# Optimization experiments

Hardware: AMD Instinct MI355X
Metric: run time of the kernel (lower is better)

Reference implementation:

```python
import jax, jax.numpy as jnp
import numpy as np

B, P_LEN, Q_LEN, HID = 8, 2048, 1024, 1024


def setup_inputs() -> dict:
    key = jax.random.key(0)
    k1, k2, k3, k4 = jax.random.split(key, 4)
    k = jax.random.normal(k1, (B, P_LEN, HID), dtype=jnp.float32)
    q = jax.random.normal(k2, (B, Q_LEN, HID), dtype=jnp.float32)
    # q_mask: True = pad token. All-valid mask (no pads) to avoid NaN rows.
    q_mask = jnp.zeros((B, Q_LEN), dtype=bool)
    # Xavier-normal-initialized Linear weights, shape [out, in] as in torch.
    std = float(np.sqrt(2.0 / (HID + HID)))
    Wk = jax.random.normal(k3, (HID, HID), dtype=jnp.float32) * std
    Wq = jax.random.normal(k4, (HID, HID), dtype=jnp.float32) * std
    return {"k": k, "q": q, "q_mask": q_mask, "Wk": Wk, "Wq": Wq}


def reference(k, q, q_mask, Wk, Wq):
    # relu-projected keys/queries (Linear has no bias)
    p_key = jax.nn.relu(jnp.einsum('bpd,hd->bph', k, Wk))   # [B, p_len, hid]
    q_key = jax.nn.relu(jnp.einsum('bqd,hd->bqh', q, Wq))   # [B, q_len, hid]
    scores = jnp.einsum('bph,bqh->bpq', p_key, q_key)        # [B, p_len, q_len]
    scores = jnp.where(q_mask[:, None, :], -jnp.inf, scores)
    alphas = jax.nn.softmax(scores, axis=-1)                 # [B, p_len, q_len]
    ctx = jnp.einsum('bpq,bqd->bpd', alphas, q)              # [B, p_len, q_dim]
    return ctx, alphas
```

## Files before the change

kernel.cpp:

```cpp
#include <hip/hip_runtime.h>
#include <hip/hip_bf16.h>
#include <math.h>


typedef _Float16 v8h __attribute__((ext_vector_type(8)));
typedef _Float16 v4h __attribute__((ext_vector_type(4)));
typedef float v4f __attribute__((ext_vector_type(4)));

#define AS1C(p) ((const __attribute__((address_space(1))) void*)(p))
#define AS3(p)  ((__attribute__((address_space(3))) void*)(p))
#define MFMA16 __builtin_amdgcn_mfma_f32_16x16x32_f16

__global__ __launch_bounds__(512) void fused_attn(
    const _Float16* __restrict__ k16,
    const _Float16* __restrict__ Wk16,
    const _Float16* __restrict__ qkey16,
    const _Float16* __restrict__ qT16,
    const unsigned char* __restrict__ qmask,
    float* __restrict__ ctx,
    float* __restrict__ alphas)
{
  extern __shared__ _Float16 lds[];
  _Float16* Pk   = lds;
  _Float16* Sbuf = lds + 65536;
  float*    red1 = (float*)(lds + 73728);
  float*    red2 = (float*)(lds + 74752);

  const int bz   = blockIdx.x & 7;
  const int pblk = blockIdx.x >> 3;
  const int p0   = pblk * 64;

  const int t  = threadIdx.x;
  const int l  = t & 63;
  const int w  = t >> 6;
  const int fr = l & 15;
  const int fq = l >> 4;
  const int w128 = w * 128;
  const int sa0 = (fq ^ (fr & 7)) * 8;
  const int sa1 = ((4 + fq) ^ (fr & 7)) * 8;

  const int trow = t >> 3;
  const int tswz = ((t & 7) ^ (trow & 7)) * 8;

  const _Float16* Kst = k16 + ((long long)(bz * 2048 + p0 + trow)) * 1024 + tswz;
  const _Float16* qkb = qkey16 + (long long)bz * 1048576;
  const _Float16* qTb = qT16   + (long long)bz * 1048576;
  float* ctxb = ctx    + (long long)(bz * 2048 + p0) * 1024;
  float* alpb = alphas + (long long)(bz * 2048 + p0) * 1024;
  const unsigned char* mskb = qmask + bz * 1024;

  {
    v4f acc0[8][4];
#pragma unroll
    for (int i = 0; i < 8; ++i)
#pragma unroll
      for (int j = 0; j < 4; ++j)
        acc0[i][j] = (v4f){0.f, 0.f, 0.f, 0.f};

#define STAGE0(kt) __builtin_amdgcn_global_load_lds( \
      AS1C(Kst + ((long long)(kt) << 6)), AS3(Sbuf + (((kt) & 1) << 12) + t * 8), 16, 0, 0)

    STAGE0(0);
    for (int kt = 0; kt < 16; ++kt) {
      if (kt < 15) {
        STAGE0(kt + 1);
        asm volatile("s_waitcnt vmcnt(1)" ::: "memory");
      } else {
        asm volatile("s_waitcnt vmcnt(0)" ::: "memory");
      }
      __builtin_amdgcn_sched_barrier(0);
      __builtin_amdgcn_s_barrier();
      asm volatile("" ::: "memory");

      const _Float16* Bs = Sbuf + ((kt & 1) << 12);
      v8h b0[4], b1[4];
#pragma unroll
      for (int j = 0; j < 4; ++j) {
        b0[j] = *(const v8h*)&Bs[(j * 16 + fr) * 64 + sa0];
        b1[j] = *(const v8h*)&Bs[(j * 16 + fr) * 64 + sa1];
      }
#pragma unroll
      for (int i = 0; i < 8; ++i) {
        const v8h a0 = *(const v8h*)&Wk16[(long long)(w128 + i * 16 + fr) * 1024 + kt * 64 + fq * 8];
        const v8h a1 = *(const v8h*)&Wk16[(long long)(w128 + i * 16 + fr) * 1024 + kt * 64 + 32 + fq * 8];
#pragma unroll
        for (int j = 0; j < 4; ++j) {
          acc0[i][j] = MFMA16(a0, b0[j], acc0[i][j], 0, 0, 0);
          acc0[i][j] = MFMA16(a1, b1[j], acc0[i][j], 0, 0, 0);
        }
      }
      asm volatile("s_waitcnt lgkmcnt(0)" ::: "memory");
      __builtin_amdgcn_sched_barrier(0);
      __builtin_amdgcn_s_barrier();
    }
#undef STAGE0

#pragma unroll
    for (int i = 0; i < 8; ++i) {
#pragma unroll
      for (int j = 0; j < 4; ++j) {
        v4f v = acc0[i][j];
        v4h h4 = {(_Float16)fmaxf(v[0], 0.f), (_Float16)fmaxf(v[1], 0.f),
                  (_Float16)fmaxf(v[2], 0.f), (_Float16)fmaxf(v[3], 0.f)};
        const int p   = j * 16 + fr;
        const int s16 = w * 16 + i * 2 + (fq >> 1);
        const int phys = (s16 & ~7) | ((s16 & 7) ^ (p & 7));
        *(v4h*)&Pk[p * 1024 + phys * 8 + (fq & 1) * 4] = h4;
      }
    }
    __syncthreads();
  }

  float M4[4], IV[4];
  {
    v4f acc[8][4];
#pragma unroll
    for (int i = 0; i < 8; ++i)
#pragma unroll
      for (int j = 0; j < 4; ++j)
        acc[i][j] = (v4f){0.f, 0.f, 0.f, 0.f};

    for (int kt = 0; kt < 16; ++kt) {
      v8h pb0[4], pb1[4];
#pragma unroll
      for (int j = 0; j < 4; ++j) {
        pb0[j] = *(const v8h*)&Pk[(j * 16 + fr) * 1024 + kt * 64 + sa0];
        pb1[j] = *(const v8h*)&Pk[(j * 16 + fr) * 1024 + kt * 64 + sa1];
      }
#pragma unroll
      for (int i = 0; i < 8; ++i) {
        const v8h a0 = *(const v8h*)&qkb[(long long)(w128 + i * 16 + fr) * 1024 + kt * 64 + fq * 8];
        const v8h a1 = *(const v8h*)&qkb[(long long)(w128 + i * 16 + fr) * 1024 + kt * 64 + 32 + fq * 8];
#pragma unroll
        for (int j = 0; j < 4; ++j) {
          acc[i][j] = MFMA16(a0, pb0[j], acc[i][j], 0, 0, 0);
          acc[i][j] = MFMA16(a1, pb1[j], acc[i][j], 0, 0, 0);
        }
      }
    }

#pragma unroll
    for (int i = 0; i < 8; ++i) {
      const unsigned m4 = *(const unsigned*)&mskb[w128 + i * 16 + fq * 4];
      if (m4) {
#pragma unroll
        for (int r = 0; r < 4; ++r)
          if ((m4 >> (8 * r)) & 0xFF) {
#pragma unroll
            for (int j = 0; j < 4; ++j) acc[i][j][r] = -INFINITY;
          }
      }
    }

#pragma unroll
    for (int j = 0; j < 4; ++j) {
      float pm = -INFINITY;
#pragma unroll
      for (int i = 0; i < 8; ++i) {
        pm = fmaxf(pm, fmaxf(fmaxf(acc[i][j][0], acc[i][j][1]),
                             fmaxf(acc[i][j][2], acc[i][j][3])));
      }
      pm = fmaxf(pm, __shfl_xor(pm, 16, 64));
      pm = fmaxf(pm, __shfl_xor(pm, 32, 64));
      if (fq == 0) red1[(j * 16 + fr) * 8 + w] = pm;
    }
    __syncthreads();
#pragma unroll
    for (int j = 0; j < 4; ++j) {
      const float* r = &red1[(j * 16 + fr) * 8];
      M4[j] = fmaxf(fmaxf(fmaxf(r[0], r[1]), fmaxf(r[2], r[3])),
                    fmaxf(fmaxf(r[4], r[5]), fmaxf(r[6], r[7])));
    }

#pragma unroll
    for (int j = 0; j < 4; ++j) {
      float ps = 0.f;
#pragma unroll
      for (int i = 0; i < 8; ++i) {
#pragma unroll
        for (int r = 0; r < 4; ++r) {
          const float e = __expf(acc[i][j][r] - M4[j]);
          acc[i][j][r] = e;
          ps += e;
        }
      }
      ps += __shfl_xor(ps, 16, 64);
      ps += __shfl_xor(ps, 32, 64);
      if (fq == 0) red2[(j * 16 + fr) * 8 + w] = ps;
    }
    __syncthreads();
#pragma unroll
    for (int j = 0; j < 4; ++j) {
      const float* r = &red2[(j * 16 + fr) * 8];
      IV[j] = 1.f / (r[0] + r[1] + r[2] + r[3] + r[4] + r[5] + r[6] + r[7]);
    }

#pragma unroll
    for (int i = 0; i < 8; ++i) {
#pragma unroll
      for (int j = 0; j < 4; ++j) {
        float4 o;
        o.x = acc[i][j][0] * IV[j];
        o.y = acc[i][j][1] * IV[j];
        o.z = acc[i][j][2] * IV[j];
        o.w = acc[i][j][3] * IV[j];
        const int p = j * 16 + fr;
        *(float4*)&alpb[(long long)p * 1024 + w128 + i * 16 + fq * 4] = o;
        v4h h4 = {(_Float16)o.x, (_Float16)o.y, (_Float16)o.z, (_Float16)o.w};
        const int s16  = w * 16 + i * 2 + (fq >> 1);
        const int phys = (s16 & ~7) | ((s16 & 7) ^ (p & 7));
        *(v4h*)&Pk[p * 1024 + phys * 8 + (fq & 1) * 4] = h4;
      }
    }
    __syncthreads();
  }

  {
    v4f acc2[4][8];
#pragma unroll
    for (int i = 0; i < 4; ++i)
#pragma unroll
      for (int j = 0; j < 8; ++j)
        acc2[i][j] = (v4f){0.f, 0.f, 0.f, 0.f};

    for (int kt = 0; kt < 16; ++kt) {
      v8h pa0[4], pa1[4];
#pragma unroll
      for (int i = 0; i < 4; ++i) {
        pa0[i] = *(const v8h*)&Pk[(i * 16 + fr) * 1024 + kt * 64 + sa0];
        pa1[i] = *(const v8h*)&Pk[(i * 16 + fr) * 1024 + kt * 64 + sa1];
      }
#pragma unroll
      for (int j = 0; j < 8; ++j) {
        const v8h b0 = *(const v8h*)&qTb[(long long)(w128 + j * 16 + fr) * 1024 + kt * 64 + fq * 8];
        const v8h b1 = *(const v8h*)&qTb[(long long)(w128 + j * 16 + fr) * 1024 + kt * 64 + 32 + fq * 8];
#pragma unroll
        for (int i = 0; i < 4; ++i) {
          acc2[i][j] = MFMA16(pa0[i], b0, acc2[i][j], 0, 0, 0);
          acc2[i][j] = MFMA16(pa1[i], b1, acc2[i][j], 0, 0, 0);
        }
      }
    }

#pragma unroll
    for (int i = 0; i < 4; ++i) {
#pragma unroll
      for (int j = 0; j < 8; ++j) {
#pragma unroll
        for (int r = 0; r < 4; ++r) {
          ctxb[(long long)(i * 16 + fq * 4 + r) * 1024 + w128 + j * 16 + fr] = acc2[i][j][r];
        }
      }
    }
  }
}

__global__ __launch_bounds__(256) void gemm_nt_f16_128(
    const _Float16* __restrict__ A, const _Float16* __restrict__ B,
    float* __restrict__ Cf, _Float16* __restrict__ Ch,
    int N, int K, int Mtiles, int Ntiles,
    long long sA, long long sB, long long sC, int relu)
{
  extern __shared__ _Float16 lds[];

  const int nwg = gridDim.x;
  const int cpx = nwg >> 3;
  const int bid = (blockIdx.x & 7) * cpx + (blockIdx.x >> 3);
  const int nt  = bid % Ntiles;
  const int mt  = (bid / Ntiles) % Mtiles;
  const int bz  = bid / (Mtiles * Ntiles);

  A += (long long)bz * sA;
  const _Float16* Bp = B + (long long)bz * sB;

  const int m0 = mt * 128;
  const int n0 = nt * 128;
  const int t  = threadIdx.x;
  const int l  = t & 63;
  const int w  = t >> 6;
  const int wm = (w >> 1) * 64;
  const int wn = (w & 1) * 64;
  const int fr = l & 15;
  const int fq = l >> 4;
  const int r3 = fr & 7;
  const int sa0 = (fq ^ r3) * 8;
  const int sa1 = ((4 + fq) ^ r3) * 8;

  const int trow = t >> 3;
  const int tswz = ((t & 7) ^ (trow & 7)) * 8;

  const _Float16* Ast = A  + (long long)(m0 + trow) * K + tswz;
  const _Float16* Bst = Bp + (long long)(n0 + trow) * K + tswz;

  v4f acc[4][4];
#pragma unroll
  for (int i = 0; i < 4; ++i)
#pragma unroll
    for (int j = 0; j < 4; ++j)
      acc[i][j] = (v4f){0.f, 0.f, 0.f, 0.f};

  const int NT = K >> 6;

#define STAGE(kt) do {                                                                   \
    _Float16* s_ = lds + (((kt) & 1) << 14);                                             \
    const long long ko_ = (long long)((kt) << 6);                                        \
    __builtin_amdgcn_global_load_lds(AS1C(Ast + ko_),            AS3(s_ +         t * 8), 16, 0, 0); \
    __builtin_amdgcn_global_load_lds(AS1C(Ast + 32LL * K + ko_), AS3(s_ +  2048 + t * 8), 16, 0, 0); \
    __builtin_amdgcn_global_load_lds(AS1C(Ast + 64LL * K + ko_), AS3(s_ +  4096 + t * 8), 16, 0, 0); \
    __builtin_amdgcn_global_load_lds(AS1C(Ast + 96LL * K + ko_), AS3(s_ +  6144 + t * 8), 16, 0, 0); \
    __builtin_amdgcn_global_load_lds(AS1C(Bst + ko_),            AS3(s_ +  8192 + t * 8), 16, 0, 0); \
    __builtin_amdgcn_global_load_lds(AS1C(Bst + 32LL * K + ko_), AS3(s_ + 10240 + t * 8), 16, 0, 0); \
    __builtin_amdgcn_global_load_lds(AS1C(Bst + 64LL * K + ko_), AS3(s_ + 12288 + t * 8), 16, 0, 0); \
    __builtin_amdgcn_global_load_lds(AS1C(Bst + 96LL * K + ko_), AS3(s_ + 14336 + t * 8), 16, 0, 0); \
  } while (0)

  STAGE(0);

  for (int kt = 0; kt < NT; ++kt) {
    if (kt + 1 < NT) {
      STAGE(kt + 1);
      asm volatile("s_waitcnt vmcnt(8)" ::: "memory");
    } else {
      asm volatile("s_waitcnt vmcnt(0)" ::: "memory");
    }
    __builtin_amdgcn_sched_barrier(0);
    __builtin_amdgcn_s_barrier();
    asm volatile("" ::: "memory");

    const _Float16* Ab = lds + ((kt & 1) << 14);
    const _Float16* Bb = Ab + 8192;

    v8h a0[4], a1[4], b0[4], b1[4];
#pragma unroll
    for (int i = 0; i < 4; ++i) {
      a0[i] = *(const v8h*)&Ab[(wm + i * 16 + fr) * 64 + sa0];
      a1[i] = *(const v8h*)&Ab[(wm + i * 16 + fr) * 64 + sa1];
    }
#pragma unroll
    for (int j = 0; j < 2; ++j) {
      b0[j] = *(const v8h*)&Bb[(wn + j * 16 + fr) * 64 + sa0];
      b1[j] = *(const v8h*)&Bb[(wn + j * 16 + fr) * 64 + sa1];
    }
    __builtin_amdgcn_s_setprio(1);
#pragma unroll
    for (int i = 0; i < 4; ++i)
#pragma unroll
      for (int j = 0; j < 2; ++j) {
        acc[i][j] = MFMA16(a0[i], b0[j], acc[i][j], 0, 0, 0);
        acc[i][j] = MFMA16(a1[i], b1[j], acc[i][j], 0, 0, 0);
      }
    __builtin_amdgcn_s_setprio(0);

#pragma unroll
    for (int j = 2; j < 4; ++j) {
      b0[j] = *(const v8h*)&Bb[(wn + j * 16 + fr) * 64 + sa0];
      b1[j] = *(const v8h*)&Bb[(wn + j * 16 + fr) * 64 + sa1];
    }
    __builtin_amdgcn_s_setprio(1);
#pragma unroll
    for (int i = 0; i < 4; ++i)
#pragma unroll
      for (int j = 2; j < 4; ++j) {
        acc[i][j] = MFMA16(a0[i], b0[j], acc[i][j], 0, 0, 0);
        acc[i][j] = MFMA16(a1[i], b1[j], acc[i][j], 0, 0, 0);
      }
    __builtin_amdgcn_s_setprio(0);

    asm volatile("s_waitcnt lgkmcnt(0)" ::: "memory");
    __builtin_amdgcn_sched_barrier(0);
    __builtin_amdgcn_s_barrier();
  }
#undef STAGE

  float* Cfb = Cf ? Cf + (long long)bz * sC : nullptr;
  _Float16* Chb = Ch ? Ch + (long long)bz * sC : nullptr;
#pragma unroll
  for (int i = 0; i < 4; ++i) {
#pragma unroll
    for (int j = 0; j < 4; ++j) {
#pragma unroll
      for (int r = 0; r < 4; ++r) {
        const int row = m0 + wm + i * 16 + fq * 4 + r;
        const int col = n0 + wn + j * 16 + fr;
        float v = acc[i][j][r];
        if (relu) v = fmaxf(v, 0.f);
        if (Cfb) Cfb[(long long)row * N + col] = v;
        if (Chb) Chb[(long long)row * N + col] = (_Float16)v;
      }
    }
  }
}

__global__ __launch_bounds__(256) void convert_all_kernel(
    const float* __restrict__ s0, _Float16* __restrict__ d0, int b0,
    const float* __restrict__ s1, _Float16* __restrict__ d1, int b1,
    const float* __restrict__ s2, _Float16* __restrict__ d2, int b2,
    const float* __restrict__ s3, _Float16* __restrict__ d3)
{
  int blk = blockIdx.x;
  const float* src;
  _Float16* dst;
  if (blk < b0)           { src = s0; dst = d0; }
  else if (blk < b0 + b1) { src = s1; dst = d1; blk -= b0; }
  else if (blk < b0 + b1 + b2) { src = s2; dst = d2; blk -= b0 + b1; }
  else                    { src = s3; dst = d3; blk -= b0 + b1 + b2; }
  const long long i = ((long long)blk * 256 + threadIdx.x) * 4;
  const float4 v = *(const float4*)(src + i);
  v4h o = {(_Float16)v.x, (_Float16)v.y, (_Float16)v.z, (_Float16)v.w};
  *(v4h*)(dst + i) = o;
}

__global__ __launch_bounds__(256) void transpose_f16_kernel(
    const float* __restrict__ q, _Float16* __restrict__ qT, int Q, int H)
{
  __shared__ float tile[64][65];
  const float* qb = q + (long long)blockIdx.z * Q * H;
  _Float16* qTb = qT + (long long)blockIdx.z * H * Q;
  const int q0 = blockIdx.x * 64, h0 = blockIdx.y * 64;
  const int t = threadIdx.x;
  const int tr = t >> 4, tc = (t & 15) << 2;
#pragma unroll
  for (int i = 0; i < 4; ++i) {
    const float4 v = *(const float4*)(qb + (long long)(q0 + tr + i * 16) * H + h0 + tc);
    tile[tr + i * 16][tc + 0] = v.x;
    tile[tr + i * 16][tc + 1] = v.y;
    tile[tr + i * 16][tc + 2] = v.z;
    tile[tr + i * 16][tc + 3] = v.w;
  }
  __syncthreads();
#pragma unroll
  for (int i = 0; i < 4; ++i) {
    const int hl = tr + i * 16;
    const int ql = tc;
    v4h o = {(_Float16)tile[ql + 0][hl], (_Float16)tile[ql + 1][hl],
             (_Float16)tile[ql + 2][hl], (_Float16)tile[ql + 3][hl]};
    *(v4h*)(qTb + (long long)(h0 + hl) * Q + q0 + ql) = o;
  }
}

extern "C" void kernel_launch(void* const* d_in, const int* in_sizes, int n_in,
                              void* d_out, int out_size, void* d_ws, size_t ws_size,
                              hipStream_t stream)
{
  const int B = 8, P = 2048, Q = 1024, H = 1024;
  const float* k  = (const float*)d_in[0];
  const float* q  = (const float*)d_in[1];
  const unsigned char* qmask = (const unsigned char*)d_in[2];
  const float* Wk = (const float*)d_in[3];
  const float* Wq = (const float*)d_in[4];

  float* ctx    = (float*)d_out;
  float* alphas = ctx + (size_t)B * P * H;

  char* wsb = (char*)d_ws;
  _Float16* qkey16 = (_Float16*)(wsb);
  _Float16* k16    = (_Float16*)(wsb + 16777216);
  _Float16* q16    = (_Float16*)(wsb + 16777216 + 33554432);
  _Float16* qT16   = q16;
  _Float16* Wk16   = (_Float16*)(wsb + 67108864);
  _Float16* Wq16   = (_Float16*)(wsb + 69206016);

  const long long nK = (long long)B * P * H;
  const long long nQ = (long long)B * Q * H;
  const long long nW = (long long)H * H;

  const int bK = (int)(nK / 1024), bQ = (int)(nQ / 1024), bW = (int)(nW / 1024);
  convert_all_kernel<<<bK + bQ + 2 * bW, 256, 0, stream>>>(
      k, k16, bK, q, q16, bQ, Wk, Wk16, bW, Wq, Wq16);

  gemm_nt_f16_128<<<64 * 8, 256, 65536, stream>>>(
      q16, Wq16, nullptr, qkey16, H, H, 64, 8, 0LL, 0LL, 0LL, 1);

  transpose_f16_kernel<<<dim3(Q / 64, H / 64, B), 256, 0, stream>>>(q, qT16, Q, H);

  fused_attn<<<256, 512, 151552, stream>>>(
      k16, Wk16, qkey16, qT16, qmask, ctx, alphas);
}
```

Before: 461.5 us.

## Register double-buffer global operand loads across all three fused GEMM phases

```diff
diff --git a/kernel.cpp b/kernel.cpp
--- a/kernel.cpp
+++ b/kernel.cpp
@@ -10,6 +10,7 @@
 #define AS1C(p) ((const __attribute__((address_space(1))) void*)(p))
 #define AS3(p)  ((__attribute__((address_space(3))) void*)(p))
 #define MFMA16 __builtin_amdgcn_mfma_f32_16x16x32_f16
+#define SB0 __builtin_amdgcn_sched_barrier(0)
 
 __global__ __launch_bounds__(512) void fused_attn(
     const _Float16* __restrict__ k16,
@@ -22,9 +23,8 @@
 {
   extern __shared__ _Float16 lds[];
   _Float16* Pk   = lds;
-  _Float16* Sbuf = lds + 65536;
-  float*    red1 = (float*)(lds + 73728);
-  float*    red2 = (float*)(lds + 74752);
+  float*    red1 = (float*)(lds + 65536);
+  float*    red2 = (float*)(lds + 66560);
 
   const int bz   = blockIdx.x & 7;
   const int pblk = blockIdx.x >> 3;
@@ -39,10 +39,7 @@
   const int sa0 = (fq ^ (fr & 7)) * 8;
   const int sa1 = ((4 + fq) ^ (fr & 7)) * 8;
 
-  const int trow = t >> 3;
-  const int tswz = ((t & 7) ^ (trow & 7)) * 8;
-
-  const _Float16* Kst = k16 + ((long long)(bz * 2048 + p0 + trow)) * 1024 + tswz;
+  const _Float16* kb  = k16    + (long long)(bz * 2048 + p0) * 1024;
   const _Float16* qkb = qkey16 + (long long)bz * 1048576;
   const _Float16* qTb = qT16   + (long long)bz * 1048576;
   float* ctxb = ctx    + (long long)(bz * 2048 + p0) * 1024;
@@ -57,43 +54,30 @@
       for (int j = 0; j < 4; ++j)
         acc0[i][j] = (v4f){0.f, 0.f, 0.f, 0.f};
 
-#define STAGE0(kt) __builtin_amdgcn_global_load_lds( \
-      AS1C(Kst + ((long long)(kt) << 6)), AS3(Sbuf + (((kt) & 1) << 12) + t * 8), 16, 0, 0)
-
-    STAGE0(0);
-    for (int kt = 0; kt < 16; ++kt) {
-      if (kt < 15) {
-        STAGE0(kt + 1);
-        asm volatile("s_waitcnt vmcnt(1)" ::: "memory");
-      } else {
-        asm volatile("s_waitcnt vmcnt(0)" ::: "memory");
-      }
-      __builtin_amdgcn_sched_barrier(0);
-      __builtin_amdgcn_s_barrier();
-      asm volatile("" ::: "memory");
-
-      const _Float16* Bs = Sbuf + ((kt & 1) << 12);
-      v8h b0[4], b1[4];
-#pragma unroll
-      for (int j = 0; j < 4; ++j) {
-        b0[j] = *(const v8h*)&Bs[(j * 16 + fr) * 64 + sa0];
-        b1[j] = *(const v8h*)&Bs[(j * 16 + fr) * 64 + sa1];
-      }
-#pragma unroll
-      for (int i = 0; i < 8; ++i) {
-        const v8h a0 = *(const v8h*)&Wk16[(long long)(w128 + i * 16 + fr) * 1024 + kt * 64 + fq * 8];
-        const v8h a1 = *(const v8h*)&Wk16[(long long)(w128 + i * 16 + fr) * 1024 + kt * 64 + 32 + fq * 8];
-#pragma unroll
-        for (int j = 0; j < 4; ++j) {
-          acc0[i][j] = MFMA16(a0, b0[j], acc0[i][j], 0, 0, 0);
-          acc0[i][j] = MFMA16(a1, b1[j], acc0[i][j], 0, 0, 0);
-        }
-      }
-      asm volatile("s_waitcnt lgkmcnt(0)" ::: "memory");
-      __builtin_amdgcn_sched_barrier(0);
-      __builtin_amdgcn_s_barrier();
-    }
-#undef STAGE0
+    v8h wA[8], wB[8], kA[4], kB[4];
+
+#define WK_LD(buf, kt, h) { _Pragma("unroll")                                              \
+    for (int i_ = 0; i_ < 8; ++i_)                                                         \
+      buf[i_] = *(const v8h*)&Wk16[(long long)(w128 + i_ * 16 + fr) * 1024 + (kt) * 64 + (h) * 32 + fq * 8]; }
+#define KK_LD(buf, kt, h) { _Pragma("unroll")                                              \
+    for (int j_ = 0; j_ < 4; ++j_)                                                         \
+      buf[j_] = *(const v8h*)&kb[(long long)(j_ * 16 + fr) * 1024 + (kt) * 64 + (h) * 32 + fq * 8]; }
+#define P0_MM(wa, ka) { _Pragma("unroll")                                                  \
+    for (int i_ = 0; i_ < 8; ++i_) { _Pragma("unroll")                                     \
+      for (int j_ = 0; j_ < 4; ++j_)                                                       \
+        acc0[i_][j_] = MFMA16(wa[i_], ka[j_], acc0[i_][j_], 0, 0, 0); } }
+
+    WK_LD(wA, 0, 0); KK_LD(kA, 0, 0);
+    for (int kt = 0; kt < 16; kt += 2) {
+      WK_LD(wB, kt, 1);     KK_LD(kB, kt, 1);     SB0;  P0_MM(wA, kA);
+      WK_LD(wA, kt + 1, 0); KK_LD(kA, kt + 1, 0); SB0;  P0_MM(wB, kB);
+      WK_LD(wB, kt + 1, 1); KK_LD(kB, kt + 1, 1); SB0;  P0_MM(wA, kA);
+      if (kt + 2 < 16) { WK_LD(wA, kt + 2, 0); KK_LD(kA, kt + 2, 0); }
+      SB0;  P0_MM(wB, kB);
+    }
+#undef WK_LD
+#undef KK_LD
+#undef P0_MM
 
 #pragma unroll
     for (int i = 0; i < 8; ++i) {
@@ -102,8 +86,8 @@
         v4f v = acc0[i][j];
         v4h h4 = {(_Float16)fmaxf(v[0], 0.f), (_Float16)fmaxf(v[1], 0.f),
                   (_Float16)fmaxf(v[2], 0.f), (_Float16)fmaxf(v[3], 0.f)};
-        const int p   = j * 16 + fr;
-        const int s16 = w * 16 + i * 2 + (fq >> 1);
+        const int p    = j * 16 + fr;
+        const int s16  = w * 16 + i * 2 + (fq >> 1);
         const int phys = (s16 & ~7) | ((s16 & 7) ^ (p & 7));
         *(v4h*)&Pk[p * 1024 + phys * 8 + (fq & 1) * 4] = h4;
       }
@@ -120,24 +104,30 @@
       for (int j = 0; j < 4; ++j)
         acc[i][j] = (v4f){0.f, 0.f, 0.f, 0.f};
 
-    for (int kt = 0; kt < 16; ++kt) {
-      v8h pb0[4], pb1[4];
-#pragma unroll
-      for (int j = 0; j < 4; ++j) {
-        pb0[j] = *(const v8h*)&Pk[(j * 16 + fr) * 1024 + kt * 64 + sa0];
-        pb1[j] = *(const v8h*)&Pk[(j * 16 + fr) * 1024 + kt * 64 + sa1];
-      }
-#pragma unroll
-      for (int i = 0; i < 8; ++i) {
-        const v8h a0 = *(const v8h*)&qkb[(long long)(w128 + i * 16 + fr) * 1024 + kt * 64 + fq * 8];
-        const v8h a1 = *(const v8h*)&qkb[(long long)(w128 + i * 16 + fr) * 1024 + kt * 64 + 32 + fq * 8];
-#pragma unroll
-        for (int j = 0; j < 4; ++j) {
-          acc[i][j] = MFMA16(a0, pb0[j], acc[i][j], 0, 0, 0);
-          acc[i][j] = MFMA16(a1, pb1[j], acc[i][j], 0, 0, 0);
-        }
-      }
-    }
+    v8h fA[8], fB[8], pb[4];
+
+#define QA_LD(buf, kt, h) { _Pragma("unroll")                                              \
+    for (int i_ = 0; i_ < 8; ++i_)                                                         \
+      buf[i_] = *(const v8h*)&qkb[(long long)(w128 + i_ * 16 + fr) * 1024 + (kt) * 64 + (h) * 32 + fq * 8]; }
+#define PB_RD(kt, h) { _Pragma("unroll")                                                   \
+    for (int j_ = 0; j_ < 4; ++j_)                                                         \
+      pb[j_] = *(const v8h*)&Pk[(j_ * 16 + fr) * 1024 + (kt) * 64 + ((h) ? sa1 : sa0)]; }
+#define PA_MM(fa) { _Pragma("unroll")                                                      \
+    for (int i_ = 0; i_ < 8; ++i_) { _Pragma("unroll")                                     \
+      for (int j_ = 0; j_ < 4; ++j_)                                                       \
+        acc[i_][j_] = MFMA16(fa[i_], pb[j_], acc[i_][j_], 0, 0, 0); } }
+
+    QA_LD(fA, 0, 0);
+    for (int kt = 0; kt < 16; kt += 2) {
+      QA_LD(fB, kt, 1);     SB0;  PB_RD(kt, 0);     PA_MM(fA);
+      QA_LD(fA, kt + 1, 0); SB0;  PB_RD(kt, 1);     PA_MM(fB);
+      QA_LD(fB, kt + 1, 1); SB0;  PB_RD(kt + 1, 0); PA_MM(fA);
+      if (kt + 2 < 16) QA_LD(fA, kt + 2, 0);
+      SB0;  PB_RD(kt + 1, 1); PA_MM(fB);
+    }
+#undef QA_LD
+#undef PB_RD
+#undef PA_MM
 
 #pragma unroll
     for (int i = 0; i < 8; ++i) {
@@ -223,24 +213,30 @@
       for (int j = 0; j < 8; ++j)
         acc2[i][j] = (v4f){0.f, 0.f, 0.f, 0.f};
 
-    for (int kt = 0; kt < 16; ++kt) {
-      v8h pa0[4], pa1[4];
-#pragma unroll
-      for (int i = 0; i < 4; ++i) {
-        pa0[i] = *(const v8h*)&Pk[(i * 16 + fr) * 1024 + kt * 64 + sa0];
-        pa1[i] = *(const v8h*)&Pk[(i * 16 + fr) * 1024 + kt * 64 + sa1];
-      }
-#pragma unroll
-      for (int j = 0; j < 8; ++j) {
-        const v8h b0 = *(const v8h*)&qTb[(long long)(w128 + j * 16 + fr) * 1024 + kt * 64 + fq * 8];
-        const v8h b1 = *(const v8h*)&qTb[(long long)(w128 + j * 16 + fr) * 1024 + kt * 64 + 32 + fq * 8];
-#pragma unroll
-        for (int i = 0; i < 4; ++i) {
-          acc2[i][j] = MFMA16(pa0[i], b0, acc2[i][j], 0, 0, 0);
-          acc2[i][j] = MFMA16(pa1[i], b1, acc2[i][j], 0, 0, 0);
-        }
-      }
-    }
+    v8h tA[8], tB[8], pa[4];
+
+#define QT_LD(buf, kt, h) { _Pragma("unroll")                                              \
+    for (int j_ = 0; j_ < 8; ++j_)                                                         \
+      buf[j_] = *(const v8h*)&qTb[(long long)(w128 + j_ * 16 + fr) * 1024 + (kt) * 64 + (h) * 32 + fq * 8]; }
+#define PA_RD(kt, h) { _Pragma("unroll")                                                   \
+    for (int i_ = 0; i_ < 4; ++i_)                                                         \
+      pa[i_] = *(const v8h*)&Pk[(i_ * 16 + fr) * 1024 + (kt) * 64 + ((h) ? sa1 : sa0)]; }
+#define PB_MM(tb) { _Pragma("unroll")                                                      \
+    for (int i_ = 0; i_ < 4; ++i_) { _Pragma("unroll")                                     \
+      for (int j_ = 0; j_ < 8; ++j_)                                                       \
+        acc2[i_][j_] = MFMA16(pa[i_], tb[j_], acc2[i_][j_], 0, 0, 0); } }
+
+    QT_LD(tA, 0, 0);
+    for (int kt = 0; kt < 16; kt += 2) {
+      QT_LD(tB, kt, 1);     SB0;  PA_RD(kt, 0);     PB_MM(tA);
+      QT_LD(tA, kt + 1, 0); SB0;  PA_RD(kt, 1);     PB_MM(tB);
+      QT_LD(tB, kt + 1, 1); SB0;  PA_RD(kt + 1, 0); PB_MM(tA);
+      if (kt + 2 < 16) QT_LD(tA, kt + 2, 0);
+      SB0;  PA_RD(kt + 1, 1); PB_MM(tB);
+    }
+#undef QT_LD
+#undef PA_RD
+#undef PB_MM
 
 #pragma unroll
     for (int i = 0; i < 4; ++i) {
@@ -473,6 +469,6 @@
 
   transpose_f16_kernel<<<dim3(Q / 64, H / 64, B), 256, 0, stream>>>(q, qT16, Q, H);
 
-  fused_attn<<<256, 512, 151552, stream>>>(
+  fused_attn<<<256, 512, 135168, stream>>>(
       k16, Wk16, qkey16, qT16, qmask, ctx, alphas);
 }
```

Result: slower. 624.5 us (+35.3%).
